# Optimization experiments

Hardware: AMD Instinct MI355X
Metric: run time of the kernel (lower is better)

The kernel has to match this reference:

```python
import jax, jax.numpy as jnp
import numpy as np
import math

D_MODEL = 512
DIM_K = 512
DIM_V = 512
N_HEADS = 8


def setup_inputs() -> dict:
    key = jax.random.key(0)
    ks = jax.random.split(key, 12)
    B, S = 2, 2048
    sc = 1.0 / math.sqrt(D_MODEL)
    return {
        "x": jax.random.normal(ks[0], (B, S, D_MODEL), dtype=jnp.float32),
        "y": jax.random.normal(ks[1], (B, S, D_MODEL), dtype=jnp.float32),
        # weights stored [in, out] so linear is x @ W + b
        "Wq": jax.random.normal(ks[2], (D_MODEL, DIM_K), dtype=jnp.float32) * sc,
        "bq": jnp.zeros((DIM_K,), dtype=jnp.float32),
        "Wk": jax.random.normal(ks[3], (D_MODEL, DIM_K), dtype=jnp.float32) * sc,
        "bk": jnp.zeros((DIM_K,), dtype=jnp.float32),
        "Wv": jax.random.normal(ks[4], (D_MODEL, DIM_V), dtype=jnp.float32) * sc,
        "bv": jnp.zeros((DIM_V,), dtype=jnp.float32),
        "Wo": jax.random.normal(ks[5], (DIM_V, D_MODEL), dtype=jnp.float32) * sc,
        "bo": jnp.zeros((D_MODEL,), dtype=jnp.float32),
    }


def reference(x, y, Wq, bq, Wk, bk, Wv, bv, Wo, bo):
    B, S, _ = x.shape
    H = N_HEADS
    Dh = DIM_K // H
    Dvh = DIM_V // H
    norm = 1.0 / math.sqrt(D_MODEL)  # note: original scales by 1/sqrt(d_model)

    # torch: q(x).reshape(-1, B, S, Dh) -> heads on leading dim (row-major)
    Q = (x @ Wq + bq).reshape(-1, B, S, Dh)      # [H,B,S,Dh]
    K = (y @ Wk + bk).reshape(-1, B, S, Dh)      # [H,B,S,Dh]
    V = (y @ Wv + bv).reshape(-1, B, S, Dvh)     # [H,B,S,Dvh]

    scores = jnp.einsum('hbqd,hbkd->hbqk', Q, K) * norm  # [H,B,S,S]

    # median-threshold mask: torch.median on even n returns lower middle value
    med_idx = (S - 1) // 2
    thre = jnp.sort(scores, axis=-1)[..., med_idx:med_idx + 1]  # [H,B,S,1]
    masked = scores - thre <= 0  # mask where score <= median
    scores = jnp.where(masked, -jnp.inf, scores)

    attn = jax.nn.softmax(scores, axis=-1)
    # dropout omitted (deterministic / eval mode)
    out = jnp.einsum('hbqk,hbkd->hbqd', attn, V)  # [H,B,S,Dvh]
    out = out.reshape(B, S, -1)                   # faithful row-major reshape
    return out @ Wo + bo
```

## Files before the change

### kernel.cpp

```cpp
#include <hip/hip_runtime.h>
#include <hip/hip_bf16.h>
#include <stdint.h>

#define SEQ    2048
#define DMODEL 512
#define NPANEL 16
#define NORM   0.044194173824159216f

typedef _Float16 f16;
typedef __attribute__((ext_vector_type(8))) _Float16 half8;
typedef __attribute__((ext_vector_type(2))) _Float16 half2v;
typedef __attribute__((ext_vector_type(4))) float f32x4;
typedef __attribute__((ext_vector_type(4))) unsigned int u32x4;

__device__ __forceinline__ unsigned umin2(unsigned a, unsigned b){ return a<b?a:b; }
__device__ __forceinline__ unsigned umax2(unsigned a, unsigned b){ return a>b?a:b; }

__global__ __launch_bounds__(256) void k_cvt(const float4* __restrict__ x,
                                             const float4* __restrict__ y,
                                             f16* __restrict__ xh, f16* __restrict__ xl,
                                             f16* __restrict__ yh, f16* __restrict__ yl){
  int i = blockIdx.x*256 + threadIdx.x;
  float4 a = x[i]; float4 b = y[i];
  half2v h0 = {(f16)a.x, (f16)a.y}, h1 = {(f16)a.z, (f16)a.w};
  *(half2v*)(xh + i*4)     = h0; *(half2v*)(xh + i*4 + 2) = h1;
  half2v l0 = {(f16)(a.x-(float)h0[0]), (f16)(a.y-(float)h0[1])};
  half2v l1 = {(f16)(a.z-(float)h1[0]), (f16)(a.w-(float)h1[1])};
  *(half2v*)(xl + i*4)     = l0; *(half2v*)(xl + i*4 + 2) = l1;
  half2v g0 = {(f16)b.x, (f16)b.y}, g1 = {(f16)b.z, (f16)b.w};
  *(half2v*)(yh + i*4)     = g0; *(half2v*)(yh + i*4 + 2) = g1;
  half2v m0 = {(f16)(b.x-(float)g0[0]), (f16)(b.y-(float)g0[1])};
  half2v m1 = {(f16)(b.z-(float)g1[0]), (f16)(b.w-(float)g1[1])};
  *(half2v*)(yl + i*4)     = m0; *(half2v*)(yl + i*4 + 2) = m1;
}

__global__ __launch_bounds__(256) void k_wt(const float* __restrict__ Wq, const float* __restrict__ Wk,
                                            const float* __restrict__ Wv, const float* __restrict__ Wo,
                                            f16* __restrict__ Wth, f16* __restrict__ Wtl){
  int z = blockIdx.z;
  const float* W = (z==0)?Wq:(z==1)?Wk:(z==2)?Wv:Wo;
  __shared__ float tile[64][65];
  int k0 = blockIdx.x*64, n0 = blockIdx.y*64;
  #pragma unroll
  for (int i = 0; i < 16; ++i){
    int s = threadIdx.x + i*256; int kl2 = s>>6, nl = s&63;
    tile[kl2][nl] = W[(k0+kl2)*512 + (n0+nl)];
  }
  __syncthreads();
  #pragma unroll
  for (int i = 0; i < 16; ++i){
    int s = threadIdx.x + i*256; int nl = s>>6, kl2 = s&63;
    float v = tile[kl2][nl];
    f16 h = (f16)v;
    int idx = z*262144 + (n0+nl)*512 + (k0+kl2);
    Wth[idx] = h;
    Wtl[idx] = (f16)(v - (float)h);
  }
}

template<int FINAL>
__global__ __launch_bounds__(256) void k_gemm(const f16* __restrict__ Ah0, const f16* __restrict__ Al0,
                                              const f16* __restrict__ Ah1, const f16* __restrict__ Al1,
                                              const f16* __restrict__ Wh, const f16* __restrict__ Wl,
                                              const float* __restrict__ b0, const float* __restrict__ b1,
                                              const float* __restrict__ b2,
                                              f16* __restrict__ Oq, float* __restrict__ Of){
  int z = blockIdx.z;
  const f16* A  = (z==0) ? Ah0 : Ah1;
  const f16* Alp= (z==0) ? Al0 : Al1;
  const f16* Bh = Wh + z*262144;
  const f16* Bl = Wl + z*262144;
  const float* bias = (z==0)?b0:(z==1)?b1:b2;
  const bool split = (FINAL==0) && (z<2);
  int m0 = blockIdx.x*128, n0 = blockIdx.y*128;

  __shared__ f16 Ahs[128][40], Bhs[128][40], Als[128][40], Bls[128][40];

  int t = threadIdx.x, l = t&63, w = t>>6;
  int wr = w>>1, wc = w&1;
  int lr = l&15, lk = l>>4;

  f32x4 acc[4][4];
  #pragma unroll
  for (int i=0;i<4;++i)
    #pragma unroll
    for (int j=0;j<4;++j) acc[i][j] = (f32x4){0.f,0.f,0.f,0.f};

  for (int ks = 0; ks < 16; ++ks){
    int k0 = ks*32;
    #pragma unroll
    for (int i = 0; i < 2; ++i){
      int s = t + i*256; int r = s>>2, kc = s&3;
      *(u32x4*)(&Ahs[r][kc*8]) = *(const u32x4*)(A   + (m0+r)*512 + k0 + kc*8);
      *(u32x4*)(&Bhs[r][kc*8]) = *(const u32x4*)(Bh  + (n0+r)*512 + k0 + kc*8);
      if (split){
        *(u32x4*)(&Als[r][kc*8]) = *(const u32x4*)(Alp + (m0+r)*512 + k0 + kc*8);
        *(u32x4*)(&Bls[r][kc*8]) = *(const u32x4*)(Bl  + (n0+r)*512 + k0 + kc*8);
      }
    }
    __syncthreads();
    half8 ah[4], bh2[4], al2[4], bl2[4];
    #pragma unroll
    for (int tm = 0; tm < 4; ++tm) ah[tm]  = *(const half8*)(&Ahs[wr*64 + tm*16 + lr][lk*8]);
    #pragma unroll
    for (int tn = 0; tn < 4; ++tn) bh2[tn] = *(const half8*)(&Bhs[wc*64 + tn*16 + lr][lk*8]);
    if (split){
      #pragma unroll
      for (int tm = 0; tm < 4; ++tm) al2[tm] = *(const half8*)(&Als[wr*64 + tm*16 + lr][lk*8]);
      #pragma unroll
      for (int tn = 0; tn < 4; ++tn) bl2[tn] = *(const half8*)(&Bls[wc*64 + tn*16 + lr][lk*8]);
    }
    #pragma unroll
    for (int tm = 0; tm < 4; ++tm)
      #pragma unroll
      for (int tn = 0; tn < 4; ++tn){
        acc[tm][tn] = __builtin_amdgcn_mfma_f32_16x16x32_f16(ah[tm], bh2[tn], acc[tm][tn], 0,0,0);
        if (split){
          acc[tm][tn] = __builtin_amdgcn_mfma_f32_16x16x32_f16(ah[tm], bl2[tn], acc[tm][tn], 0,0,0);
          acc[tm][tn] = __builtin_amdgcn_mfma_f32_16x16x32_f16(al2[tm], bh2[tn], acc[tm][tn], 0,0,0);
        }
      }
    __syncthreads();
  }

  #pragma unroll
  for (int tn = 0; tn < 4; ++tn){
    int n_g = n0 + wc*64 + tn*16 + lr;
    float bv = bias[n_g];
    #pragma unroll
    for (int tm = 0; tm < 4; ++tm){
      #pragma unroll
      for (int r = 0; r < 4; ++r){
        int m_g = m0 + wr*64 + tm*16 + lk*4 + r;
        float v = acc[tm][tn][r] + bv;
        size_t idx = (size_t)m_g*512 + n_g;
        if (FINAL){
          Of[idx] = v;
        } else if (z < 2){
          f16 h = (f16)v;
          Oq[(size_t)z*4194304 + idx] = h;
          Oq[(size_t)z*4194304 + 2097152 + idx] = (f16)(v - (float)h);
        } else {
          Oq[(size_t)4*2097152 + idx] = (f16)v;
        }
      }
    }
  }
}

__global__ __launch_bounds__(256) void k_vt(const unsigned short* __restrict__ V, unsigned short* __restrict__ Vt){
  int p = blockIdx.y;
  int t = threadIdx.x;
  int d = t & 63, sc = t >> 6;
  int s0b = blockIdx.x*32 + sc*8;
  const unsigned short* Vp = V + p*131072;
  unsigned short* Vtp = Vt + p*131072;
  typedef __attribute__((ext_vector_type(8))) short short8;
  short8 vv;
  #pragma unroll
  for (int j = 0; j < 8; ++j) vv[j] = (short)Vp[(s0b + j)*64 + d];
  *(short8*)(Vtp + d*2048 + s0b) = vv;
}

__global__ __launch_bounds__(512, 4) void k_attn(const f16* __restrict__ Qh, const f16* __restrict__ Ql,
                                                 const f16* __restrict__ Kh, const f16* __restrict__ Kl,
                                                 const f16* __restrict__ Vt, f16* __restrict__ O){
  extern __shared__ char scb[];
  __shared__ float rzs[16];
  __shared__ float red[1024];
  int p = blockIdx.x, qt = blockIdx.y;
  int s0 = qt*16;
  const f16* Qhp = Qh + p*131072;
  const f16* Qlp = Ql + p*131072;
  const f16* Khp = Kh + p*131072;
  const f16* Klp = Kl + p*131072;
  const f16* Vtp = Vt + p*131072;
  int t = threadIdx.x, l = t&63, w = t>>6;
  int lr = l&15, lk = l>>4;

  half8 qh[2], ql[2];
  #pragma unroll
  for (int f = 0; f < 2; ++f){
    qh[f] = *(const half8*)(Qhp + (s0+lr)*64 + f*32 + lk*8);
    ql[f] = *(const half8*)(Qlp + (s0+lr)*64 + f*32 + lk*8);
  }

  unsigned ovA0[16], ovA1[16];

  #pragma unroll 1
  for (int ph = 0; ph < 2; ++ph){
    const f16* ka = Khp + ((ph<<10) + w*128 + lr)*64 + lk*8;
    const f16* la = Klp + ((ph<<10) + w*128 + lr)*64 + lk*8;
    int n = w*128 + lr;
    #pragma unroll 1
    for (int ct = 0; ct < 8; ++ct){
      half8 kb0 = *(const half8*)(ka);
      half8 kb1 = *(const half8*)(ka + 32);
      half8 lb0 = *(const half8*)(la);
      half8 lb1 = *(const half8*)(la + 32);
      f32x4 c1 = (f32x4){0.f,0.f,0.f,0.f};
      f32x4 c2 = (f32x4){0.f,0.f,0.f,0.f};
      f32x4 c3 = (f32x4){0.f,0.f,0.f,0.f};
      c1 = __builtin_amdgcn_mfma_f32_16x16x32_f16(qh[0], kb0, c1, 0,0,0);
      c2 = __builtin_amdgcn_mfma_f32_16x16x32_f16(qh[0], lb0, c2, 0,0,0);
      c3 = __builtin_amdgcn_mfma_f32_16x16x32_f16(ql[0], kb0, c3, 0,0,0);
      c1 = __builtin_amdgcn_mfma_f32_16x16x32_f16(qh[1], kb1, c1, 0,0,0);
      c2 = __builtin_amdgcn_mfma_f32_16x16x32_f16(qh[1], lb1, c2, 0,0,0);
      c3 = __builtin_amdgcn_mfma_f32_16x16x32_f16(ql[1], kb1, c3, 0,0,0);
      #pragma unroll
      for (int r = 0; r < 4; ++r){
        int row = lk*4 + r;
        *(float*)(scb + row*4096 + (((unsigned)(n*4)) ^ ((unsigned)(lk<<6)))) = c1[r] + c2[r] + c3[r];
      }
      ka += 1024; la += 1024; n += 16;
    }
    __syncthreads();
    if (ph == 0){
      unsigned C = ((unsigned)((w>>1)&3))<<6;
      const char* rb0 = scb + (w*2)*4096;
      const char* rb1 = rb0 + 4096;
      #pragma unroll
      for (int j = 0; j < 16; ++j){
        unsigned off = (((unsigned)((l + j*64)*4)) ^ C);
        unsigned u0 = *(const unsigned*)(rb0 + off);
        unsigned u1 = *(const unsigned*)(rb1 + off);
        ovA0[j] = ((int)u0 < 0) ? ~u0 : (u0 | 0x80000000u);
        ovA1[j] = ((int)u1 < 0) ? ~u1 : (u1 | 0x80000000u);
      }
      __syncthreads();
    }
  }

  #pragma unroll 1
  for (int rr = 0; rr < 2; ++rr){
    int row = w*2 + rr;
    const char* rb = scb + row*4096;
    unsigned C = ((unsigned)((row>>2)&3))<<6;
    unsigned o2[16];
    #pragma unroll
    for (int j = 0; j < 16; ++j){
      unsigned u = *(const unsigned*)(rb + (((unsigned)((l + j*64)*4)) ^ C));
      o2[j] = ((int)u < 0) ? ~u : (u | 0x80000000u);
    }
    unsigned umn = 0xFFFFFFFFu, umx = 0u;
    #pragma unroll
    for (int j = 0; j < 16; ++j){
      unsigned a = (rr==0) ? ovA0[j] : ovA1[j];
      umn = umin2(umn, umin2(a, o2[j]));
      umx = umax2(umax2(umx, a), o2[j]);
    }
    #pragma unroll
    for (int off2 = 1; off2 < 64; off2 <<= 1){
      umn = umin2(umn, (unsigned)__shfl_xor((int)umn, off2));
      umx = umax2(umx, (unsigned)__shfl_xor((int)umx, off2));
    }
    unsigned thr;
    {
      unsigned L = umn, R = umx;
      #pragma unroll 1
      for (;;){
        if (L >= R){ thr = R; break; }
        unsigned mid = L + ((R - L) >> 1);
        int c = 0;
        #pragma unroll
        for (int j = 0; j < 16; ++j){
          unsigned a = (rr==0) ? ovA0[j] : ovA1[j];
          c += (int)__popcll(__ballot(a <= mid));
          c += (int)__popcll(__ballot(o2[j] <= mid));
        }
        if (c == 1024){ thr = mid; break; }
        if (c > 1024) R = mid; else L = mid + 1;
      }
    }
    unsigned bmx = (umx & 0x80000000u) ? (umx & 0x7FFFFFFFu) : ~umx;
    float mx = __uint_as_float(bmx);
    float zs = 0.f;
    unsigned g = ((unsigned)(row & 7)) << 4;
    char* pb = scb + row*4096;
    #pragma unroll
    for (int j = 0; j < 32; ++j){
      unsigned a = (j < 16) ? ((rr==0) ? ovA0[j] : ovA1[j]) : o2[j-16];
      unsigned b = (a & 0x80000000u) ? (a & 0x7FFFFFFFu) : ~a;
      float v = __uint_as_float(b);
      float wgt = (a <= thr) ? 0.f : __expf((v - mx) * NORM);
      zs += wgt;
      unsigned col = (unsigned)((j & 15)*64 + l + (j >> 4)*1024);
      *(f16*)(pb + ((col*2) ^ g)) = (f16)wgt;
    }
    #pragma unroll
    for (int off2 = 1; off2 < 64; off2 <<= 1) zs += __shfl_xor(zs, off2);
    if (l == 0) rzs[row] = 1.f / zs;
  }
  __syncthreads();

  int oc = w & 3, kh2 = w >> 2;
  const f16* vb = Vtp + (oc*16 + lr)*2048 + kh2*1024 + lk*8;
  const char* pbase = scb + lr*4096;
  unsigned pswz = ((unsigned)(lr & 7)) << 4;
  unsigned pk = (unsigned)(kh2*1024 + lk*8);
  f32x4 o0 = (f32x4){0.f,0.f,0.f,0.f};
  f32x4 o1 = (f32x4){0.f,0.f,0.f,0.f};
  #pragma unroll 1
  for (int it = 0; it < 16; ++it){
    half8 pa0 = *(const half8*)(pbase + (((pk)*2) ^ pswz));
    half8 vb0 = *(const half8*)(vb);
    half8 pa1 = *(const half8*)(pbase + (((pk + 32)*2) ^ pswz));
    half8 vb1 = *(const half8*)(vb + 32);
    o0 = __builtin_amdgcn_mfma_f32_16x16x32_f16(pa0, vb0, o0, 0,0,0);
    o1 = __builtin_amdgcn_mfma_f32_16x16x32_f16(pa1, vb1, o1, 0,0,0);
    pk += 64; vb += 64;
  }
  f32x4 oa;
  #pragma unroll
  for (int r = 0; r < 4; ++r) oa[r] = o0[r] + o1[r];
  if (kh2 == 1){
    #pragma unroll
    for (int r = 0; r < 4; ++r) red[oc*256 + (lk*4+r)*16 + lr] = oa[r];
  }
  __syncthreads();
  if (kh2 == 0){
    #pragma unroll
    for (int r = 0; r < 4; ++r){
      int row = lk*4 + r;
      float v = (oa[r] + red[oc*256 + row*16 + lr]) * rzs[row];
      O[p*131072 + (s0+row)*64 + oc*16 + lr] = (f16)v;
    }
  }
}

extern "C" void kernel_launch(void* const* d_in, const int* in_sizes, int n_in,
                              void* d_out, int out_size, void* d_ws, size_t ws_size,
                              hipStream_t stream) {
  const float* x  = (const float*)d_in[0];
  const float* y  = (const float*)d_in[1];
  const float* Wq = (const float*)d_in[2];
  const float* bq = (const float*)d_in[3];
  const float* Wk = (const float*)d_in[4];
  const float* bk = (const float*)d_in[5];
  const float* Wv = (const float*)d_in[6];
  const float* bv = (const float*)d_in[7];
  const float* Wo = (const float*)d_in[8];
  const float* bo = (const float*)d_in[9];

  f16* ws = (f16*)d_ws;
  f16* xh  = ws;
  f16* xl  = ws + 2097152;
  f16* yh  = ws + 4194304;
  f16* yl  = ws + 6291456;
  f16* Wth = ws + 8388608;
  f16* Wtl = ws + 9437184;
  f16* QKV = ws + 10485760;
  f16* Vt  = ws;
  f16* Ob  = ws + 2097152;

  (void)hipFuncSetAttribute(reinterpret_cast<const void*>(k_attn),
                            hipFuncAttributeMaxDynamicSharedMemorySize, 65536);

  k_cvt<<<2048, 256, 0, stream>>>((const float4*)x, (const float4*)y, xh, xl, yh, yl);
  k_wt<<<dim3(8,8,4), 256, 0, stream>>>(Wq, Wk, Wv, Wo, Wth, Wtl);
  k_gemm<0><<<dim3(32,4,3), 256, 0, stream>>>(xh, xl, yh, yl, Wth, Wtl, bq, bk, bv, QKV, nullptr);
  k_vt<<<dim3(64,16), 256, 0, stream>>>((const unsigned short*)(QKV + 4*2097152), (unsigned short*)Vt);
  k_attn<<<dim3(16,128), 512, 65536, stream>>>(QKV, QKV + 2097152, QKV + 2*2097152, QKV + 3*2097152, Vt, Ob);
  k_gemm<1><<<dim3(32,4,1), 256, 0, stream>>>(Ob, Ob, Ob, Ob, Wth + 3*262144, Wtl, bo, bo, bo, nullptr, (float*)d_out);
}
```

Before: 287.1 us.

## Halve attention query tile to 8 rows with 256-thread blocks

Shrinks each attention block from 16 to 8 query rows, with 4 waves instead of 8 and half the dynamic LDS, and doubles the grid. Each wave now covers twice as many key columns. The P·V stage runs over the full key length per wave, which removes the cross-wave reduction buffer and one barrier. The aim is higher occupancy and less synchronisation. The cost is that the 16x16 MFMAs now compute duplicated rows, and K/V is streamed twice as often overall.

Measured after the change: 457.6 us. +59.4%, slower.

```diff
diff --git a/kernel.cpp b/kernel.cpp
--- a/kernel.cpp
+++ b/kernel.cpp
@@ -162,14 +162,13 @@
   *(short8*)(Vtp + d*2048 + s0b) = vv;
 }
 
-__global__ __launch_bounds__(512, 4) void k_attn(const f16* __restrict__ Qh, const f16* __restrict__ Ql,
+__global__ __launch_bounds__(256, 4) void k_attn(const f16* __restrict__ Qh, const f16* __restrict__ Ql,
                                                  const f16* __restrict__ Kh, const f16* __restrict__ Kl,
                                                  const f16* __restrict__ Vt, f16* __restrict__ O){
   extern __shared__ char scb[];
-  __shared__ float rzs[16];
-  __shared__ float red[1024];
+  __shared__ float rzs[8];
   int p = blockIdx.x, qt = blockIdx.y;
-  int s0 = qt*16;
+  int s0 = qt*8;
   const f16* Qhp = Qh + p*131072;
   const f16* Qlp = Ql + p*131072;
   const f16* Khp = Kh + p*131072;
@@ -177,23 +176,24 @@
   const f16* Vtp = Vt + p*131072;
   int t = threadIdx.x, l = t&63, w = t>>6;
   int lr = l&15, lk = l>>4;
+  int qr = lr & 7;
 
   half8 qh[2], ql[2];
   #pragma unroll
   for (int f = 0; f < 2; ++f){
-    qh[f] = *(const half8*)(Qhp + (s0+lr)*64 + f*32 + lk*8);
-    ql[f] = *(const half8*)(Qlp + (s0+lr)*64 + f*32 + lk*8);
+    qh[f] = *(const half8*)(Qhp + (s0+qr)*64 + f*32 + lk*8);
+    ql[f] = *(const half8*)(Qlp + (s0+qr)*64 + f*32 + lk*8);
   }
 
   unsigned ovA0[16], ovA1[16];
 
   #pragma unroll 1
   for (int ph = 0; ph < 2; ++ph){
-    const f16* ka = Khp + ((ph<<10) + w*128 + lr)*64 + lk*8;
-    const f16* la = Klp + ((ph<<10) + w*128 + lr)*64 + lk*8;
-    int n = w*128 + lr;
+    const f16* ka = Khp + ((ph<<10) + w*256 + lr)*64 + lk*8;
+    const f16* la = Klp + ((ph<<10) + w*256 + lr)*64 + lk*8;
+    int n = w*256 + lr;
     #pragma unroll 1
-    for (int ct = 0; ct < 8; ++ct){
+    for (int ct = 0; ct < 16; ++ct){
       half8 kb0 = *(const half8*)(ka);
       half8 kb1 = *(const half8*)(ka + 32);
       half8 lb0 = *(const half8*)(la);
@@ -207,10 +207,12 @@
       c1 = __builtin_amdgcn_mfma_f32_16x16x32_f16(qh[1], kb1, c1, 0,0,0);
       c2 = __builtin_amdgcn_mfma_f32_16x16x32_f16(qh[1], lb1, c2, 0,0,0);
       c3 = __builtin_amdgcn_mfma_f32_16x16x32_f16(ql[1], kb1, c3, 0,0,0);
-      #pragma unroll
-      for (int r = 0; r < 4; ++r){
-        int row = lk*4 + r;
-        *(float*)(scb + row*4096 + (((unsigned)(n*4)) ^ ((unsigned)(lk<<6)))) = c1[r] + c2[r] + c3[r];
+      if (lk < 2){
+        #pragma unroll
+        for (int r = 0; r < 4; ++r){
+          int row = lk*4 + r;
+          *(float*)(scb + row*4096 + (((unsigned)(n*4)) ^ ((unsigned)(lk<<6)))) = c1[r] + c2[r] + c3[r];
+        }
       }
       ka += 1024; la += 1024; n += 16;
     }
@@ -293,16 +295,16 @@
   }
   __syncthreads();
 
-  int oc = w & 3, kh2 = w >> 2;
-  const f16* vb = Vtp + (oc*16 + lr)*2048 + kh2*1024 + lk*8;
-  const char* pbase = scb + lr*4096;
-  unsigned pswz = ((unsigned)(lr & 7)) << 4;
-  unsigned pk = (unsigned)(kh2*1024 + lk*8);
+  int oc = w;
+  const f16* vb = Vtp + (oc*16 + lr)*2048 + lk*8;
+  const char* pbase = scb + qr*4096;
+  unsigned pswz = ((unsigned)qr) << 4;
+  unsigned pk = (unsigned)(lk*8);
   f32x4 o0 = (f32x4){0.f,0.f,0.f,0.f};
   f32x4 o1 = (f32x4){0.f,0.f,0.f,0.f};
   #pragma unroll 1
-  for (int it = 0; it < 16; ++it){
-    half8 pa0 = *(const half8*)(pbase + (((pk)*2) ^ pswz));
+  for (int it = 0; it < 32; ++it){
+    half8 pa0 = *(const half8*)(pbase + ((pk*2) ^ pswz));
     half8 vb0 = *(const half8*)(vb);
     half8 pa1 = *(const half8*)(pbase + (((pk + 32)*2) ^ pswz));
     half8 vb1 = *(const half8*)(vb + 32);
@@ -310,19 +312,11 @@
     o1 = __builtin_amdgcn_mfma_f32_16x16x32_f16(pa1, vb1, o1, 0,0,0);
     pk += 64; vb += 64;
   }
-  f32x4 oa;
-  #pragma unroll
-  for (int r = 0; r < 4; ++r) oa[r] = o0[r] + o1[r];
-  if (kh2 == 1){
-    #pragma unroll
-    for (int r = 0; r < 4; ++r) red[oc*256 + (lk*4+r)*16 + lr] = oa[r];
-  }
-  __syncthreads();
-  if (kh2 == 0){
+  if (lk < 2){
     #pragma unroll
     for (int r = 0; r < 4; ++r){
       int row = lk*4 + r;
-      float v = (oa[r] + red[oc*256 + row*16 + lr]) * rzs[row];
+      float v = (o0[r] + o1[r]) * rzs[row];
       O[p*131072 + (s0+row)*64 + oc*16 + lr] = (f16)v;
     }
   }
@@ -354,12 +348,12 @@
   f16* Ob  = ws + 2097152;
 
   (void)hipFuncSetAttribute(reinterpret_cast<const void*>(k_attn),
-                            hipFuncAttributeMaxDynamicSharedMemorySize, 65536);
+                            hipFuncAttributeMaxDynamicSharedMemorySize, 32768);
 
   k_cvt<<<2048, 256, 0, stream>>>((const float4*)x, (const float4*)y, xh, xl, yh, yl);
   k_wt<<<dim3(8,8,4), 256, 0, stream>>>(Wq, Wk, Wv, Wo, Wth, Wtl);
   k_gemm<0><<<dim3(32,4,3), 256, 0, stream>>>(xh, xl, yh, yl, Wth, Wtl, bq, bk, bv, QKV, nullptr);
   k_vt<<<dim3(64,16), 256, 0, stream>>>((const unsigned short*)(QKV + 4*2097152), (unsigned short*)Vt);
-  k_attn<<<dim3(16,128), 512, 65536, stream>>>(QKV, QKV + 2097152, QKV + 2*2097152, QKV + 3*2097152, Vt, Ob);
+  k_attn<<<dim3(16,256), 256, 32768, stream>>>(QKV, QKV + 2097152, QKV + 2*2097152, QKV + 3*2097152, Vt, Ob);
   k_gemm<1><<<dim3(32,4,1), 256, 0, stream>>>(Ob, Ob, Ob, Ob, Wth + 3*262144, Wtl, bo, bo, bo, nullptr, (float*)d_out);
 }
```
